# Kernel optimization log

Hardware: AMD Instinct MI355X
Metric: run time of the kernel (lower is better)

## Reference

```python
import jax, jax.numpy as jnp
import numpy as np

B, N, C, H = 8192, 36, 128, 8
HD = C // H  # 16
FOCUS = 3
EPS = 1e-4


def setup_inputs() -> dict:
    key = jax.random.key(0)
    ks = jax.random.split(key, 10)
    x = jax.random.normal(ks[0], (B, N, C), dtype=jnp.float32)
    pos = jax.random.normal(ks[1], (B, N, C), dtype=jnp.float32)
    mask = jax.random.randint(ks[2], (B, N), 0, 2).astype(jnp.float32)
    coords = jax.random.randint(ks[3], (B * N, 4), 0, 8).astype(jnp.int64)
    voxel_inds = jax.random.permutation(ks[4], B * N).reshape(B, N).astype(jnp.int64)
    s = 0.02
    qk_w = jax.random.normal(ks[5], (C, 2 * C), dtype=jnp.float32) * s
    qk_b = jnp.zeros((2 * C,), dtype=jnp.float32)
    v_w = jax.random.normal(ks[6], (C, C), dtype=jnp.float32) * s
    v_b = jnp.zeros((C,), dtype=jnp.float32)
    proj_w = jax.random.normal(ks[7], (C, C), dtype=jnp.float32) * s
    proj_b = jnp.zeros((C,), dtype=jnp.float32)
    return {"x": x, "pos": pos, "mask": mask, "qk_w": qk_w, "qk_b": qk_b,
            "v_w": v_w, "v_b": v_b, "proj_w": proj_w, "proj_b": proj_b,
            "coords": coords, "voxel_inds": voxel_inds}


def reference(x, pos, mask, qk_w, qk_b, v_w, v_b, proj_w, proj_b, coords, voxel_inds):
    b, n, c = x.shape
    qk = (x + pos) @ qk_w + qk_b                      # (B,N,2C)
    q, k = qk[..., :c], qk[..., c:]
    v = x @ v_w + v_b                                 # (B,N,C)
    k = k * mask[..., None]
    # split heads -> (B,H,N,HD)
    q = q.reshape(b, n, H, HD).transpose(0, 2, 1, 3)
    k = k.reshape(b, n, H, HD).transpose(0, 2, 1, 3)
    v = v.reshape(b, n, H, HD).transpose(0, 2, 1, 3)
    # focusing power
    q = q ** FOCUS
    k = k ** FOCUS
    # q normalized per-token over channels; k normalized per-channel over tokens
    # (original rearranges k to (bh, c, n) before norm(dim=-1))
    q = q / (EPS + jnp.linalg.norm(q, axis=-1, keepdims=True))
    k = k / (EPS + jnp.linalg.norm(k, axis=2, keepdims=True))
    # linear attention: kv = k^T v (HD x HD), then q @ kv
    kv = jnp.einsum('bhnc,bhnd->bhcd', k, v)          # (B,H,HD,HD)
    out = jnp.einsum('bhnc,bhcd->bhnd', q, kv)        # (B,H,N,HD)
    out = out.transpose(0, 2, 1, 3).reshape(b, n, c)  # (B,N,C)
    num = jnp.sum(mask, axis=-1, keepdims=True)       # (B,1)
    out = out / (num[..., None] + EPS)
    # inverse-permutation gather: perm[voxel_inds.flat] = arange
    flat = voxel_inds.reshape(-1)
    M = coords.shape[0]
    perm = jnp.zeros((M,), dtype=flat.dtype).at[flat].set(
        jnp.arange(M, dtype=flat.dtype))
    out = out.reshape(-1, c)[perm]                    # (M,C)
    out = out @ proj_w + proj_b
    return out
```

## Files before the change

kernel.cpp:

```cpp
#include <hip/hip_runtime.h>

typedef __bf16 bf16x8 __attribute__((ext_vector_type(8)));
typedef float f32x4 __attribute__((ext_vector_type(4)));

#define Bdim 8192
#define NBLK 512
#define NBATCH 16
#define Nn 36
#define Cc 128
#define EPSf 1e-4f

#define WS_QK_HI 0
#define WS_QK_LO 32768
#define WS_V_HI  65536
#define WS_P_HI  81920

#define OFF_XH   0
#define OFF_PH   12288
#define OFF_PL   24576
#define OFF_KT   36864
#define OFF_VT   50176
#define OFF_QO   63488
#define OFF_MASK 75776
#define OFF_INN  76160
#define LDS_BYTES 76288

__device__ inline uint bfh(float f) {
    __bf16 h = (__bf16)f;
    return (uint)(*(const ushort*)&h);
}
__device__ inline uint bfl(float f) {
    float hf = (float)((__bf16)f);
    __bf16 l = (__bf16)(f - hf);
    return (uint)(*(const ushort*)&l);
}
__device__ inline uint pk2h(float a, float b) { return bfh(a) | (bfh(b) << 16); }
__device__ inline uint pk2l(float a, float b) { return bfl(a) | (bfl(b) << 16); }

union U8 { bf16x8 v; uint u[4]; };

__device__ __forceinline__ void put3(char* L, int idx, float4 xv, float4 pv) {
    int n = idx >> 5, c4 = (idx & 31) << 2;
    float s0 = xv.x + pv.x, s1 = xv.y + pv.y;
    float s2 = xv.z + pv.z, s3 = xv.w + pv.w;
    uint ba = (uint)n * 256u + (((uint)(c4 * 2)) ^ (((uint)n & 15u) << 4));
    *(uint2*)(L + OFF_XH + ba) = make_uint2(pk2h(xv.x, xv.y), pk2h(xv.z, xv.w));
    *(uint2*)(L + OFF_PH + ba) = make_uint2(pk2h(s0, s1), pk2h(s2, s3));
    *(uint2*)(L + OFF_PL + ba) = make_uint2(pk2l(s0, s1), pk2l(s2, s3));
}

__device__ __forceinline__ void stage_batch(char* L, const float* __restrict__ x,
                                            const float* __restrict__ pos,
                                            const float* __restrict__ mask,
                                            int bb, int t, int wv, int lane, int pe) {
    const float* xg = x + (size_t)bb * (Nn * Cc);
    const float* pg = pos + (size_t)bb * (Nn * Cc);
    {
        int idx = t;
        int n = idx >> 5, c4 = (idx & 31) << 2;
        put3(L, idx, *(const float4*)(xg + n * Cc + c4), *(const float4*)(pg + n * Cc + c4));
    }
    {
        int idx = t + 512;
        int n = idx >> 5, c4 = (idx & 31) << 2;
        put3(L, idx, *(const float4*)(xg + n * Cc + c4), *(const float4*)(pg + n * Cc + c4));
    }
    if (t < 128) {
        int idx = t + 1024;
        int n = idx >> 5, c4 = (idx & 31) << 2;
        put3(L, idx, *(const float4*)(xg + n * Cc + c4), *(const float4*)(pg + n * Cc + c4));
    }
    float mvv = (t < Nn) ? mask[(size_t)bb * Nn + t] : 0.f;
    if (t < 48) ((float*)(L + OFF_MASK))[pe * 48 + t] = mvv;
    if (wv == 0) {
        float s = mvv;
        s += __shfl_xor(s, 1);  s += __shfl_xor(s, 2);
        s += __shfl_xor(s, 4);  s += __shfl_xor(s, 8);
        s += __shfl_xor(s, 16); s += __shfl_xor(s, 32);
        if (lane == 0) ((float*)(L + OFF_INN))[pe] = 1.f / (s + EPSf);
    }
}

__global__ __launch_bounds__(256)
void prep_frags(const float* __restrict__ qk_w, const float* __restrict__ v_w,
                const float* __restrict__ proj_w, ushort* __restrict__ ws)
{
    int e = blockIdx.x * 256 + threadIdx.x;
    const float* W; int N; int idx; int hi_off; int lo_off;
    if (e < 32768)      { W = qk_w;   N = 256; hi_off = WS_QK_HI; lo_off = WS_QK_LO; idx = e; }
    else if (e < 49152) { W = v_w;    N = 128; hi_off = WS_V_HI;  lo_off = -1;       idx = e - 32768; }
    else                { W = proj_w; N = 128; hi_off = WS_P_HI;  lo_off = -1;       idx = e - 49152; }
    int j    = idx & 7;
    int lane = (idx >> 3) & 63;
    int ks   = (idx >> 9) & 3;
    int ct   = idx >> 11;
    int col  = ct * 16 + (lane & 15);
    int k    = ks * 32 + (lane >> 4) * 8 + j;
    float v  = W[k * N + col];
    ws[hi_off + idx] = (ushort)bfh(v);
    if (lo_off >= 0) ws[lo_off + idx] = (ushort)bfl(v);
}

__global__ __launch_bounds__(512, 2)
void fla_mfma(const float* __restrict__ x, const float* __restrict__ pos,
              const float* __restrict__ mask, const float* __restrict__ qk_b,
              const float* __restrict__ v_b, const float* __restrict__ proj_b,
              const int* __restrict__ vox, const ushort* __restrict__ ws,
              float* __restrict__ out)
{
    __shared__ __align__(16) char lds[LDS_BYTES];
    const int t = threadIdx.x;
    const int lane = t & 63;
    const int wv = t >> 6;
    const int  rsel = lane & 15;
    const int  grp  = lane >> 4;
    const uint kgrp = (uint)grp * 8u;
    const uint sw   = ((uint)rsel) << 4;
    const int base = blockIdx.x * NBATCH;

    const int   c16 = wv * 16 + rsel;
    const float qb = qk_b[c16];
    const float kb = qk_b[Cc + c16];
    const float vb = v_b[c16];
    const float pb = proj_b[c16];

    stage_batch(lds, x, pos, mask, base, t, wv, lane, 0);
    __syncthreads();

    #pragma unroll 1
    for (int i = 0; i < NBATCH; ++i) {
        const int pe = i & 1;

        f32x4 accQ[3], accK[3];
        #pragma unroll
        for (int rt = 0; rt < 3; ++rt) {
            accQ[rt] = (f32x4){0.f, 0.f, 0.f, 0.f};
            accK[rt] = (f32x4){0.f, 0.f, 0.f, 0.f};
        }
        #pragma unroll
        for (int ks = 0; ks < 4; ++ks) {
            uint ka = (((uint)(ks * 32) + kgrp) * 2u) ^ sw;
            bf16x8 ph[3], pl[3];
            #pragma unroll
            for (int rt = 0; rt < 3; ++rt) {
                uint ba = (uint)(rt * 16 + rsel) * 256u + ka;
                ph[rt] = *(const bf16x8*)(lds + OFF_PH + ba);
                pl[rt] = *(const bf16x8*)(lds + OFF_PL + ba);
            }
            int fq = ((wv * 4 + ks) * 64 + lane) * 8;
            int fk = (((8 + wv) * 4 + ks) * 64 + lane) * 8;
            bf16x8 bqh = *(const bf16x8*)(ws + WS_QK_HI + fq);
            bf16x8 bql = *(const bf16x8*)(ws + WS_QK_LO + fq);
            bf16x8 bkh = *(const bf16x8*)(ws + WS_QK_HI + fk);
            bf16x8 bkl = *(const bf16x8*)(ws + WS_QK_LO + fk);
            #pragma unroll
            for (int rt = 0; rt < 3; ++rt) {
                accQ[rt] = __builtin_amdgcn_mfma_f32_16x16x32_bf16(ph[rt], bqh, accQ[rt], 0, 0, 0);
                accQ[rt] = __builtin_amdgcn_mfma_f32_16x16x32_bf16(ph[rt], bql, accQ[rt], 0, 0, 0);
                accQ[rt] = __builtin_amdgcn_mfma_f32_16x16x32_bf16(pl[rt], bqh, accQ[rt], 0, 0, 0);
                accK[rt] = __builtin_amdgcn_mfma_f32_16x16x32_bf16(ph[rt], bkh, accK[rt], 0, 0, 0);
                accK[rt] = __builtin_amdgcn_mfma_f32_16x16x32_bf16(ph[rt], bkl, accK[rt], 0, 0, 0);
                accK[rt] = __builtin_amdgcn_mfma_f32_16x16x32_bf16(pl[rt], bkh, accK[rt], 0, 0, 0);
            }
        }
        f32x4 accV[3];
        #pragma unroll
        for (int rt = 0; rt < 3; ++rt) accV[rt] = (f32x4){0.f, 0.f, 0.f, 0.f};
        #pragma unroll
        for (int ks = 0; ks < 4; ++ks) {
            uint ka = (((uint)(ks * 32) + kgrp) * 2u) ^ sw;
            bf16x8 xh[3];
            #pragma unroll
            for (int rt = 0; rt < 3; ++rt)
                xh[rt] = *(const bf16x8*)(lds + OFF_XH + (uint)(rt * 16 + rsel) * 256u + ka);
            int fv = ((wv * 4 + ks) * 64 + lane) * 8;
            bf16x8 bvh = *(const bf16x8*)(ws + WS_V_HI + fv);
            #pragma unroll
            for (int rt = 0; rt < 3; ++rt)
                accV[rt] = __builtin_amdgcn_mfma_f32_16x16x32_bf16(xh[rt], bvh, accV[rt], 0, 0, 0);
        }
        __syncthreads();

        {
            const float* sM = (const float*)(lds + OFF_MASK) + pe * 48;
            uint cb2 = (uint)(c16 * 2);
            #pragma unroll
            for (int rt = 0; rt < 3; ++rt) {
                #pragma unroll
                for (int r = 0; r < 4; ++r) {
                    int row = rt * 16 + grp * 4 + r;
                    if (row < Nn) {
                        float q1 = accQ[rt][r] + qb;
                        float q3 = q1 * q1 * q1;
                        uint ba = (uint)row * 256u + (cb2 ^ (((uint)row & 15u) << 4));
                        *(ushort*)(lds + OFF_QO + ba) = (ushort)bfh(q3);
                    }
                }
            }
            #pragma unroll
            for (int rt = 0; rt < 3; ++rt) {
                float k3v[4];
                #pragma unroll
                for (int r = 0; r < 4; ++r) {
                    int row = rt * 16 + grp * 4 + r;
                    float k1 = (accK[rt][r] + kb) * sM[row];
                    float k3 = k1 * k1 * k1;
                    k3v[r] = (rt == 2 && grp != 0) ? 0.f : k3;
                }
                uint addr = OFF_KT + (uint)(c16 * 52 + rt * 16 + grp * 4) * 2u;
                *(uint2*)(lds + addr) = make_uint2(pk2h(k3v[0], k3v[1]), pk2h(k3v[2], k3v[3]));
            }
        }
        #pragma unroll
        for (int rt = 0; rt < 3; ++rt) {
            float a0 = accV[rt][0] + vb, a1 = accV[rt][1] + vb;
            float a2 = accV[rt][2] + vb, a3 = accV[rt][3] + vb;
            if (rt == 2 && grp != 0) { a0 = 0.f; a1 = 0.f; a2 = 0.f; a3 = 0.f; }
            uint addr = OFF_VT + (uint)(c16 * 52 + rt * 16 + grp * 4) * 2u;
            *(uint2*)(lds + addr) = make_uint2(pk2h(a0, a1), pk2h(a2, a3));
        }

        if (i + 1 < NBATCH)
            stage_batch(lds, x, pos, mask, base + i + 1, t, wv, lane, pe ^ 1);

        f32x4 kvacc;
        {
            uint a0 = OFF_KT + (uint)(c16 * 52 + grp * 8) * 2u;
            uint b0 = OFF_VT + (uint)(c16 * 52 + grp * 8) * 2u;
            bf16x8 kA0 = *(const bf16x8*)(lds + a0);
            bf16x8 vB0 = *(const bf16x8*)(lds + b0);
            U8 kA1, vB1;
            kA1.u[0] = kA1.u[1] = kA1.u[2] = kA1.u[3] = 0u;
            vB1.u[0] = vB1.u[1] = vB1.u[2] = vB1.u[3] = 0u;
            if (grp < 2) {
                kA1.v = *(const bf16x8*)(lds + a0 + 64);
                vB1.v = *(const bf16x8*)(lds + b0 + 64);
            }
            float s = 0.f;
            #pragma unroll
            for (int j = 0; j < 8; ++j) { float q = (float)kA0[j]; s += q * q; }
            #pragma unroll
            for (int j = 0; j < 8; ++j) { float q = (float)kA1.v[j]; s += q * q; }
            s += __shfl_xor(s, 16);
            s += __shfl_xor(s, 32);
            float invkn = 1.f / (EPSf + sqrtf(s));

            kvacc = (f32x4){0.f, 0.f, 0.f, 0.f};
            kvacc = __builtin_amdgcn_mfma_f32_16x16x32_bf16(kA0, vB0, kvacc, 0, 0, 0);
            kvacc = __builtin_amdgcn_mfma_f32_16x16x32_bf16(kA1.v, vB1.v, kvacc, 0, 0, 0);
            #pragma unroll
            for (int r = 0; r < 4; ++r)
                kvacc[r] *= __shfl(invkn, grp * 4 + r);
        }

        {
            float bv[8];
            #pragma unroll
            for (int j = 0; j < 8; ++j)
                bv[j] = __shfl(kvacc[j & 3], rsel + 16 * (2 * grp + (j >> 2)));
            if (grp >= 2) {
                #pragma unroll
                for (int j = 0; j < 8; ++j) bv[j] = 0.f;
            }
            U8 bkv;
            bkv.u[0] = pk2h(bv[0], bv[1]); bkv.u[1] = pk2h(bv[2], bv[3]);
            bkv.u[2] = pk2h(bv[4], bv[5]); bkv.u[3] = pk2h(bv[6], bv[7]);

            float inn = ((const float*)(lds + OFF_INN))[pe];
            U8 aq[3];
            #pragma unroll
            for (int rt = 0; rt < 3; ++rt) {
                int row = rt * 16 + rsel;
                aq[rt].u[0] = aq[rt].u[1] = aq[rt].u[2] = aq[rt].u[3] = 0u;
                if (grp < 2 && row < Nn)
                    aq[rt].v = *(const bf16x8*)(lds + OFF_QO + (uint)row * 256u +
                                                (((uint)(wv * 32 + grp * 16)) ^ sw));
            }
            f32x4 oacc[3];
            float invn[3];
            #pragma unroll
            for (int rt = 0; rt < 3; ++rt) {
                float s = 0.f;
                #pragma unroll
                for (int j = 0; j < 8; ++j) { float q = (float)aq[rt].v[j]; s += q * q; }
                s += __shfl_xor(s, 16);
                invn[rt] = 1.f / (EPSf + sqrtf(s));
                f32x4 o = (f32x4){0.f, 0.f, 0.f, 0.f};
                o = __builtin_amdgcn_mfma_f32_16x16x32_bf16(aq[rt].v, bkv.v, o, 0, 0, 0);
                oacc[rt] = o;
            }
            uint cb2 = (uint)(c16 * 2);
            #pragma unroll
            for (int rt = 0; rt < 3; ++rt) {
                #pragma unroll
                for (int r = 0; r < 4; ++r) {
                    int rr = grp * 4 + r;
                    int row = rt * 16 + rr;
                    if (row < Nn) {
                        float fac = __shfl(invn[rt], rr) * inn;
                        float val = oacc[rt][r] * fac;
                        uint ba = (uint)row * 256u + (cb2 ^ (((uint)row & 15u) << 4));
                        *(ushort*)(lds + OFF_QO + ba) = (ushort)bfh(val);
                    }
                }
            }
        }
        __syncthreads();

        {
            f32x4 accP[3];
            #pragma unroll
            for (int rt = 0; rt < 3; ++rt) accP[rt] = (f32x4){0.f, 0.f, 0.f, 0.f};
            #pragma unroll
            for (int ks = 0; ks < 4; ++ks) {
                uint ka = (((uint)(ks * 32) + kgrp) * 2u) ^ sw;
                bf16x8 oa[3];
                #pragma unroll
                for (int rt = 0; rt < 3; ++rt)
                    oa[rt] = *(const bf16x8*)(lds + OFF_QO + (uint)(rt * 16 + rsel) * 256u + ka);
                int fp = ((wv * 4 + ks) * 64 + lane) * 8;
                bf16x8 bp = *(const bf16x8*)(ws + WS_P_HI + fp);
                #pragma unroll
                for (int rt = 0; rt < 3; ++rt)
                    accP[rt] = __builtin_amdgcn_mfma_f32_16x16x32_bf16(oa[rt], bp, accP[rt], 0, 0, 0);
            }
            const int* voxb = vox + (size_t)(base + i) * Nn;
            #pragma unroll
            for (int rt = 0; rt < 3; ++rt) {
                #pragma unroll
                for (int r = 0; r < 4; ++r) {
                    int row = rt * 16 + grp * 4 + r;
                    if (row < Nn)
                        out[(size_t)voxb[row] * Cc + c16] = accP[rt][r] + pb;
                }
            }
        }
    }
}

extern "C" void kernel_launch(void* const* d_in, const int* in_sizes, int n_in,
                              void* d_out, int out_size, void* d_ws, size_t ws_size,
                              hipStream_t stream) {
    (void)in_sizes; (void)n_in; (void)out_size; (void)ws_size;
    const float* x      = (const float*)d_in[0];
    const float* pos    = (const float*)d_in[1];
    const float* mask   = (const float*)d_in[2];
    const float* qk_w   = (const float*)d_in[3];
    const float* qk_b   = (const float*)d_in[4];
    const float* v_w    = (const float*)d_in[5];
    const float* v_b    = (const float*)d_in[6];
    const float* proj_w = (const float*)d_in[7];
    const float* proj_b = (const float*)d_in[8];
    const int*   vox    = (const int*)d_in[10];
    ushort* ws = (ushort*)d_ws;
    float* outp = (float*)d_out;

    hipLaunchKernelGGL(prep_frags, dim3(256), dim3(256), 0, stream, qk_w, v_w, proj_w, ws);
    hipLaunchKernelGGL(fla_mfma, dim3(NBLK), dim3(512), 0, stream,
                       x, pos, mask, qk_b, v_b, proj_b, vox, ws, outp);
}
```

Before: 251.8 us.

## Double-buffer LDS per batch, prefetch next batch into registers, hoist QK weight fragments

Splits LDS into two full per-batch buffers so the next batch's x/pos/mask global loads are issued at the top of each iteration into registers and written to the alternate buffer after the attention stage. This hides global load latency behind the QK/V MFMA work and drops one __syncthreads per iteration. QK weight fragments are loaded once into registers instead of per batch, and padding rows are zeroed once. In exchange LDS nearly doubles (about 152KB per block), which may cut occupancy below the two blocks per CU requested, and register pressure rises from the held prefetch and weight fragments.

```diff
diff --git a/kernel.cpp b/kernel.cpp
--- a/kernel.cpp
+++ b/kernel.cpp
@@ -22,8 +22,8 @@
 #define OFF_VT   50176
 #define OFF_QO   63488
 #define OFF_MASK 75776
-#define OFF_INN  76160
-#define LDS_BYTES 76288
+#define OFF_INN  75968
+#define AST      75984
 
 __device__ inline uint bfh(float f) {
     __bf16 h = (__bf16)f;
@@ -47,38 +47,6 @@
     *(uint2*)(L + OFF_XH + ba) = make_uint2(pk2h(xv.x, xv.y), pk2h(xv.z, xv.w));
     *(uint2*)(L + OFF_PH + ba) = make_uint2(pk2h(s0, s1), pk2h(s2, s3));
     *(uint2*)(L + OFF_PL + ba) = make_uint2(pk2l(s0, s1), pk2l(s2, s3));
-}
-
-__device__ __forceinline__ void stage_batch(char* L, const float* __restrict__ x,
-                                            const float* __restrict__ pos,
-                                            const float* __restrict__ mask,
-                                            int bb, int t, int wv, int lane, int pe) {
-    const float* xg = x + (size_t)bb * (Nn * Cc);
-    const float* pg = pos + (size_t)bb * (Nn * Cc);
-    {
-        int idx = t;
-        int n = idx >> 5, c4 = (idx & 31) << 2;
-        put3(L, idx, *(const float4*)(xg + n * Cc + c4), *(const float4*)(pg + n * Cc + c4));
-    }
-    {
-        int idx = t + 512;
-        int n = idx >> 5, c4 = (idx & 31) << 2;
-        put3(L, idx, *(const float4*)(xg + n * Cc + c4), *(const float4*)(pg + n * Cc + c4));
-    }
-    if (t < 128) {
-        int idx = t + 1024;
-        int n = idx >> 5, c4 = (idx & 31) << 2;
-        put3(L, idx, *(const float4*)(xg + n * Cc + c4), *(const float4*)(pg + n * Cc + c4));
-    }
-    float mvv = (t < Nn) ? mask[(size_t)bb * Nn + t] : 0.f;
-    if (t < 48) ((float*)(L + OFF_MASK))[pe * 48 + t] = mvv;
-    if (wv == 0) {
-        float s = mvv;
-        s += __shfl_xor(s, 1);  s += __shfl_xor(s, 2);
-        s += __shfl_xor(s, 4);  s += __shfl_xor(s, 8);
-        s += __shfl_xor(s, 16); s += __shfl_xor(s, 32);
-        if (lane == 0) ((float*)(L + OFF_INN))[pe] = 1.f / (s + EPSf);
-    }
 }
 
 __global__ __launch_bounds__(256)
@@ -108,7 +76,7 @@
               const int* __restrict__ vox, const ushort* __restrict__ ws,
               float* __restrict__ out)
 {
-    __shared__ __align__(16) char lds[LDS_BYTES];
+    __shared__ __align__(16) char lds[2][AST];
     const int t = threadIdx.x;
     const int lane = t & 63;
     const int wv = t >> 6;
@@ -124,12 +92,72 @@
     const float vb = v_b[c16];
     const float pb = proj_b[c16];
 
-    stage_batch(lds, x, pos, mask, base, t, wv, lane, 0);
+    bf16x8 BQH[4], BQL[4], BKH[4], BKL[4];
+    #pragma unroll
+    for (int ks = 0; ks < 4; ++ks) {
+        int fq = ((wv * 4 + ks) * 64 + lane) * 8;
+        int fk = (((8 + wv) * 4 + ks) * 64 + lane) * 8;
+        BQH[ks] = *(const bf16x8*)(ws + WS_QK_HI + fq);
+        BQL[ks] = *(const bf16x8*)(ws + WS_QK_LO + fq);
+        BKH[ks] = *(const bf16x8*)(ws + WS_QK_HI + fk);
+        BKL[ks] = *(const bf16x8*)(ws + WS_QK_LO + fk);
+    }
+
+    #pragma unroll
+    for (int z0 = 0; z0 < 3; ++z0) {
+        int z = t + z0 * 512;
+        int ar = z >= 768;
+        int zz = z & 767;
+        int reg = zz / 192;
+        int off = (zz % 192) * 16;
+        uint ro = (reg == 0) ? OFF_XH : (reg == 1) ? OFF_PH : (reg == 2) ? OFF_PL : OFF_QO;
+        *(uint4*)(lds[ar] + ro + 36 * 256 + off) = make_uint4(0u, 0u, 0u, 0u);
+    }
+
+    {
+        const float* xg = x + (size_t)base * (Nn * Cc);
+        const float* pg = pos + (size_t)base * (Nn * Cc);
+        { int n = t >> 5, c4 = (t & 31) << 2;
+          put3(lds[0], t, *(const float4*)(xg + n * Cc + c4), *(const float4*)(pg + n * Cc + c4)); }
+        { int idx = t + 512; int n = idx >> 5, c4 = (idx & 31) << 2;
+          put3(lds[0], idx, *(const float4*)(xg + n * Cc + c4), *(const float4*)(pg + n * Cc + c4)); }
+        if (t < 128) { int idx = t + 1024; int n = idx >> 5, c4 = (idx & 31) << 2;
+          put3(lds[0], idx, *(const float4*)(xg + n * Cc + c4), *(const float4*)(pg + n * Cc + c4)); }
+        float mvv = (t < Nn) ? mask[(size_t)base * Nn + t] : 0.f;
+        if (t < 48) ((float*)(lds[0] + OFF_MASK))[t] = mvv;
+        if (wv == 0) {
+            float s = mvv;
+            s += __shfl_xor(s, 1);  s += __shfl_xor(s, 2);
+            s += __shfl_xor(s, 4);  s += __shfl_xor(s, 8);
+            s += __shfl_xor(s, 16); s += __shfl_xor(s, 32);
+            if (lane == 0) *(float*)(lds[0] + OFF_INN) = 1.f / (s + EPSf);
+        }
+    }
     __syncthreads();
 
     #pragma unroll 1
     for (int i = 0; i < NBATCH; ++i) {
-        const int pe = i & 1;
+        char* L  = lds[i & 1];
+        char* Ln = lds[(i + 1) & 1];
+        const bool more = (i + 1 < NBATCH);
+
+        float4 lx0, lp0, lx1, lp1, lx2, lp2;
+        float lmv = 0.f;
+        if (more) {
+            const float* xg = x + (size_t)(base + i + 1) * (Nn * Cc);
+            const float* pg = pos + (size_t)(base + i + 1) * (Nn * Cc);
+            { int n = t >> 5, c4 = (t & 31) << 2;
+              lx0 = *(const float4*)(xg + n * Cc + c4);
+              lp0 = *(const float4*)(pg + n * Cc + c4); }
+            { int idx = t + 512; int n = idx >> 5, c4 = (idx & 31) << 2;
+              lx1 = *(const float4*)(xg + n * Cc + c4);
+              lp1 = *(const float4*)(pg + n * Cc + c4); }
+            if (t < 128) { int idx = t + 1024; int n = idx >> 5, c4 = (idx & 31) << 2;
+              lx2 = *(const float4*)(xg + n * Cc + c4);
+              lp2 = *(const float4*)(pg + n * Cc + c4); }
+            lmv = (t < Nn) ? mask[(size_t)(base + i + 1) * Nn + t] : 0.f;
+        }
+        __builtin_amdgcn_sched_barrier(0);
 
         f32x4 accQ[3], accK[3];
         #pragma unroll
@@ -144,23 +172,17 @@
             #pragma unroll
             for (int rt = 0; rt < 3; ++rt) {
                 uint ba = (uint)(rt * 16 + rsel) * 256u + ka;
-                ph[rt] = *(const bf16x8*)(lds + OFF_PH + ba);
-                pl[rt] = *(const bf16x8*)(lds + OFF_PL + ba);
-            }
-            int fq = ((wv * 4 + ks) * 64 + lane) * 8;
-            int fk = (((8 + wv) * 4 + ks) * 64 + lane) * 8;
-            bf16x8 bqh = *(const bf16x8*)(ws + WS_QK_HI + fq);
-            bf16x8 bql = *(const bf16x8*)(ws + WS_QK_LO + fq);
-            bf16x8 bkh = *(const bf16x8*)(ws + WS_QK_HI + fk);
-            bf16x8 bkl = *(const bf16x8*)(ws + WS_QK_LO + fk);
-            #pragma unroll
-            for (int rt = 0; rt < 3; ++rt) {
-                accQ[rt] = __builtin_amdgcn_mfma_f32_16x16x32_bf16(ph[rt], bqh, accQ[rt], 0, 0, 0);
-                accQ[rt] = __builtin_amdgcn_mfma_f32_16x16x32_bf16(ph[rt], bql, accQ[rt], 0, 0, 0);
-                accQ[rt] = __builtin_amdgcn_mfma_f32_16x16x32_bf16(pl[rt], bqh, accQ[rt], 0, 0, 0);
-                accK[rt] = __builtin_amdgcn_mfma_f32_16x16x32_bf16(ph[rt], bkh, accK[rt], 0, 0, 0);
-                accK[rt] = __builtin_amdgcn_mfma_f32_16x16x32_bf16(ph[rt], bkl, accK[rt], 0, 0, 0);
-                accK[rt] = __builtin_amdgcn_mfma_f32_16x16x32_bf16(pl[rt], bkh, accK[rt], 0, 0, 0);
+                ph[rt] = *(const bf16x8*)(L + OFF_PH + ba);
+                pl[rt] = *(const bf16x8*)(L + OFF_PL + ba);
+            }
+            #pragma unroll
+            for (int rt = 0; rt < 3; ++rt) {
+                accQ[rt] = __builtin_amdgcn_mfma_f32_16x16x32_bf16(ph[rt], BQH[ks], accQ[rt], 0, 0, 0);
+                accQ[rt] = __builtin_amdgcn_mfma_f32_16x16x32_bf16(ph[rt], BQL[ks], accQ[rt], 0, 0, 0);
+                accQ[rt] = __builtin_amdgcn_mfma_f32_16x16x32_bf16(pl[rt], BQH[ks], accQ[rt], 0, 0, 0);
+                accK[rt] = __builtin_amdgcn_mfma_f32_16x16x32_bf16(ph[rt], BKH[ks], accK[rt], 0, 0, 0);
+                accK[rt] = __builtin_amdgcn_mfma_f32_16x16x32_bf16(ph[rt], BKL[ks], accK[rt], 0, 0, 0);
+                accK[rt] = __builtin_amdgcn_mfma_f32_16x16x32_bf16(pl[rt], BKH[ks], accK[rt], 0, 0, 0);
             }
         }
         f32x4 accV[3];
@@ -172,17 +194,16 @@
             bf16x8 xh[3];
             #pragma unroll
             for (int rt = 0; rt < 3; ++rt)
-                xh[rt] = *(const bf16x8*)(lds + OFF_XH + (uint)(rt * 16 + rsel) * 256u + ka);
+                xh[rt] = *(const bf16x8*)(L + OFF_XH + (uint)(rt * 16 + rsel) * 256u + ka);
             int fv = ((wv * 4 + ks) * 64 + lane) * 8;
             bf16x8 bvh = *(const bf16x8*)(ws + WS_V_HI + fv);
             #pragma unroll
             for (int rt = 0; rt < 3; ++rt)
                 accV[rt] = __builtin_amdgcn_mfma_f32_16x16x32_bf16(xh[rt], bvh, accV[rt], 0, 0, 0);
         }
-        __syncthreads();
 
         {
-            const float* sM = (const float*)(lds + OFF_MASK) + pe * 48;
+            const float* sM = (const float*)(L + OFF_MASK);
             uint cb2 = (uint)(c16 * 2);
             #pragma unroll
             for (int rt = 0; rt < 3; ++rt) {
@@ -193,7 +214,7 @@
                         float q1 = accQ[rt][r] + qb;
                         float q3 = q1 * q1 * q1;
                         uint ba = (uint)row * 256u + (cb2 ^ (((uint)row & 15u) << 4));
-                        *(ushort*)(lds + OFF_QO + ba) = (ushort)bfh(q3);
+                        *(ushort*)(L + OFF_QO + ba) = (ushort)bfh(q3);
                     }
                 }
             }
@@ -208,7 +229,7 @@
                     k3v[r] = (rt == 2 && grp != 0) ? 0.f : k3;
                 }
                 uint addr = OFF_KT + (uint)(c16 * 52 + rt * 16 + grp * 4) * 2u;
-                *(uint2*)(lds + addr) = make_uint2(pk2h(k3v[0], k3v[1]), pk2h(k3v[2], k3v[3]));
+                *(uint2*)(L + addr) = make_uint2(pk2h(k3v[0], k3v[1]), pk2h(k3v[2], k3v[3]));
             }
         }
         #pragma unroll
@@ -217,24 +238,21 @@
             float a2 = accV[rt][2] + vb, a3 = accV[rt][3] + vb;
             if (rt == 2 && grp != 0) { a0 = 0.f; a1 = 0.f; a2 = 0.f; a3 = 0.f; }
             uint addr = OFF_VT + (uint)(c16 * 52 + rt * 16 + grp * 4) * 2u;
-            *(uint2*)(lds + addr) = make_uint2(pk2h(a0, a1), pk2h(a2, a3));
-        }
-
-        if (i + 1 < NBATCH)
-            stage_batch(lds, x, pos, mask, base + i + 1, t, wv, lane, pe ^ 1);
+            *(uint2*)(L + addr) = make_uint2(pk2h(a0, a1), pk2h(a2, a3));
+        }
 
         f32x4 kvacc;
         {
             uint a0 = OFF_KT + (uint)(c16 * 52 + grp * 8) * 2u;
             uint b0 = OFF_VT + (uint)(c16 * 52 + grp * 8) * 2u;
-            bf16x8 kA0 = *(const bf16x8*)(lds + a0);
-            bf16x8 vB0 = *(const bf16x8*)(lds + b0);
+            bf16x8 kA0 = *(const bf16x8*)(L + a0);
+            bf16x8 vB0 = *(const bf16x8*)(L + b0);
             U8 kA1, vB1;
             kA1.u[0] = kA1.u[1] = kA1.u[2] = kA1.u[3] = 0u;
             vB1.u[0] = vB1.u[1] = vB1.u[2] = vB1.u[3] = 0u;
             if (grp < 2) {
-                kA1.v = *(const bf16x8*)(lds + a0 + 64);
-                vB1.v = *(const bf16x8*)(lds + b0 + 64);
+                kA1.v = *(const bf16x8*)(L + a0 + 64);
+                vB1.v = *(const bf16x8*)(L + b0 + 64);
             }
             float s = 0.f;
             #pragma unroll
@@ -266,14 +284,14 @@
             bkv.u[0] = pk2h(bv[0], bv[1]); bkv.u[1] = pk2h(bv[2], bv[3]);
             bkv.u[2] = pk2h(bv[4], bv[5]); bkv.u[3] = pk2h(bv[6], bv[7]);
 
-            float inn = ((const float*)(lds + OFF_INN))[pe];
+            float inn = *(const float*)(L + OFF_INN);
             U8 aq[3];
             #pragma unroll
             for (int rt = 0; rt < 3; ++rt) {
                 int row = rt * 16 + rsel;
                 aq[rt].u[0] = aq[rt].u[1] = aq[rt].u[2] = aq[rt].u[3] = 0u;
                 if (grp < 2 && row < Nn)
-                    aq[rt].v = *(const bf16x8*)(lds + OFF_QO + (uint)row * 256u +
+                    aq[rt].v = *(const bf16x8*)(L + OFF_QO + (uint)row * 256u +
                                                 (((uint)(wv * 32 + grp * 16)) ^ sw));
             }
             f32x4 oacc[3];
@@ -300,9 +318,23 @@
                         float fac = __shfl(invn[rt], rr) * inn;
                         float val = oacc[rt][r] * fac;
                         uint ba = (uint)row * 256u + (cb2 ^ (((uint)row & 15u) << 4));
-                        *(ushort*)(lds + OFF_QO + ba) = (ushort)bfh(val);
+                        *(ushort*)(L + OFF_QO + ba) = (ushort)bfh(val);
                     }
                 }
+            }
+        }
+
+        if (more) {
+            put3(Ln, t, lx0, lp0);
+            put3(Ln, t + 512, lx1, lp1);
+            if (t < 128) put3(Ln, t + 1024, lx2, lp2);
+            if (t < 48) ((float*)(Ln + OFF_MASK))[t] = lmv;
+            if (wv == 0) {
+                float s = lmv;
+                s += __shfl_xor(s, 1);  s += __shfl_xor(s, 2);
+                s += __shfl_xor(s, 4);  s += __shfl_xor(s, 8);
+                s += __shfl_xor(s, 16); s += __shfl_xor(s, 32);
+                if (lane == 0) *(float*)(Ln + OFF_INN) = 1.f / (s + EPSf);
             }
         }
         __syncthreads();
@@ -317,7 +349,7 @@
                 bf16x8 oa[3];
                 #pragma unroll
                 for (int rt = 0; rt < 3; ++rt)
-                    oa[rt] = *(const bf16x8*)(lds + OFF_QO + (uint)(rt * 16 + rsel) * 256u + ka);
+                    oa[rt] = *(const bf16x8*)(L + OFF_QO + (uint)(rt * 16 + rsel) * 256u + ka);
                 int fp = ((wv * 4 + ks) * 64 + lane) * 8;
                 bf16x8 bp = *(const bf16x8*)(ws + WS_P_HI + fp);
                 #pragma unroll
```

Measured after the change: 228.6 us. -9.2%, faster.

## Process two batches per block with interleaved stages and smaller aliased LDS

Applied to the files above, without the earlier changes.

Replaces the 512-block persistent loop over 16 batches with 4096 blocks that each handle two batches. Work is split into stage lambdas that are interleaved across the two batches, so one batch's MFMA work overlaps the other's staging and epilogue. The LDS regions for the staged inputs and the K/V/Q buffers now alias, which roughly halves shared memory per batch and lets launch bounds request 4 blocks per CU. The cost is more blocks, each reloading weight fragments, and register pressure from holding two sets of accumulators.

```diff
diff --git a/kernel.cpp b/kernel.cpp
--- a/kernel.cpp
+++ b/kernel.cpp
@@ -4,8 +4,6 @@
 typedef float f32x4 __attribute__((ext_vector_type(4)));
 
 #define Bdim 8192
-#define NBLK 512
-#define NBATCH 16
 #define Nn 36
 #define Cc 128
 #define EPSf 1e-4f
@@ -18,12 +16,12 @@
 #define OFF_XH   0
 #define OFF_PH   12288
 #define OFF_PL   24576
-#define OFF_KT   36864
-#define OFF_VT   50176
-#define OFF_QO   63488
-#define OFF_MASK 75776
-#define OFF_INN  76160
-#define LDS_BYTES 76288
+#define OFF_KT   0
+#define OFF_VT   13312
+#define OFF_QO   26624
+#define OFF_MASK 38912
+#define OFF_INN  39104
+#define AST      39168
 
 __device__ inline uint bfh(float f) {
     __bf16 h = (__bf16)f;
@@ -38,48 +36,6 @@
 __device__ inline uint pk2l(float a, float b) { return bfl(a) | (bfl(b) << 16); }
 
 union U8 { bf16x8 v; uint u[4]; };
-
-__device__ __forceinline__ void put3(char* L, int idx, float4 xv, float4 pv) {
-    int n = idx >> 5, c4 = (idx & 31) << 2;
-    float s0 = xv.x + pv.x, s1 = xv.y + pv.y;
-    float s2 = xv.z + pv.z, s3 = xv.w + pv.w;
-    uint ba = (uint)n * 256u + (((uint)(c4 * 2)) ^ (((uint)n & 15u) << 4));
-    *(uint2*)(L + OFF_XH + ba) = make_uint2(pk2h(xv.x, xv.y), pk2h(xv.z, xv.w));
-    *(uint2*)(L + OFF_PH + ba) = make_uint2(pk2h(s0, s1), pk2h(s2, s3));
-    *(uint2*)(L + OFF_PL + ba) = make_uint2(pk2l(s0, s1), pk2l(s2, s3));
-}
-
-__device__ __forceinline__ void stage_batch(char* L, const float* __restrict__ x,
-                                            const float* __restrict__ pos,
-                                            const float* __restrict__ mask,
-                                            int bb, int t, int wv, int lane, int pe) {
-    const float* xg = x + (size_t)bb * (Nn * Cc);
-    const float* pg = pos + (size_t)bb * (Nn * Cc);
-    {
-        int idx = t;
-        int n = idx >> 5, c4 = (idx & 31) << 2;
-        put3(L, idx, *(const float4*)(xg + n * Cc + c4), *(const float4*)(pg + n * Cc + c4));
-    }
-    {
-        int idx = t + 512;
-        int n = idx >> 5, c4 = (idx & 31) << 2;
-        put3(L, idx, *(const float4*)(xg + n * Cc + c4), *(const float4*)(pg + n * Cc + c4));
-    }
-    if (t < 128) {
-        int idx = t + 1024;
-        int n = idx >> 5, c4 = (idx & 31) << 2;
-        put3(L, idx, *(const float4*)(xg + n * Cc + c4), *(const float4*)(pg + n * Cc + c4));
-    }
-    float mvv = (t < Nn) ? mask[(size_t)bb * Nn + t] : 0.f;
-    if (t < 48) ((float*)(L + OFF_MASK))[pe * 48 + t] = mvv;
-    if (wv == 0) {
-        float s = mvv;
-        s += __shfl_xor(s, 1);  s += __shfl_xor(s, 2);
-        s += __shfl_xor(s, 4);  s += __shfl_xor(s, 8);
-        s += __shfl_xor(s, 16); s += __shfl_xor(s, 32);
-        if (lane == 0) ((float*)(L + OFF_INN))[pe] = 1.f / (s + EPSf);
-    }
-}
 
 __global__ __launch_bounds__(256)
 void prep_frags(const float* __restrict__ qk_w, const float* __restrict__ v_w,
@@ -101,14 +57,14 @@
     if (lo_off >= 0) ws[lo_off + idx] = (ushort)bfl(v);
 }
 
-__global__ __launch_bounds__(512, 2)
+__global__ __launch_bounds__(512, 4)
 void fla_mfma(const float* __restrict__ x, const float* __restrict__ pos,
               const float* __restrict__ mask, const float* __restrict__ qk_b,
               const float* __restrict__ v_b, const float* __restrict__ proj_b,
               const int* __restrict__ vox, const ushort* __restrict__ ws,
               float* __restrict__ out)
 {
-    __shared__ __align__(16) char lds[LDS_BYTES];
+    __shared__ __align__(16) char lds[2][AST];
     const int t = threadIdx.x;
     const int lane = t & 63;
     const int wv = t >> 6;
@@ -116,7 +72,9 @@
     const int  grp  = lane >> 4;
     const uint kgrp = (uint)grp * 8u;
     const uint sw   = ((uint)rsel) << 4;
-    const int base = blockIdx.x * NBATCH;
+
+    const int b0 = blockIdx.x * 2;
+    const int b1 = b0 + 1;
 
     const int   c16 = wv * 16 + rsel;
     const float qb = qk_b[c16];
@@ -124,18 +82,42 @@
     const float vb = v_b[c16];
     const float pb = proj_b[c16];
 
-    stage_batch(lds, x, pos, mask, base, t, wv, lane, 0);
-    __syncthreads();
-
-    #pragma unroll 1
-    for (int i = 0; i < NBATCH; ++i) {
-        const int pe = i & 1;
-
-        f32x4 accQ[3], accK[3];
+    auto PA = [&](int ar, int bb) {
+        char* L = lds[ar];
+        const float* xg = x + (size_t)bb * (Nn * Cc);
+        const float* pg = pos + (size_t)bb * (Nn * Cc);
+        auto put = [&](int idx) {
+            int n = idx >> 5, c4 = (idx & 31) << 2;
+            float4 xv = *(const float4*)(xg + n * Cc + c4);
+            float4 pv = *(const float4*)(pg + n * Cc + c4);
+            float s0 = xv.x + pv.x, s1 = xv.y + pv.y;
+            float s2 = xv.z + pv.z, s3 = xv.w + pv.w;
+            uint ba = (uint)n * 256u + (((uint)(c4 * 2)) ^ (((uint)n & 15u) << 4));
+            *(uint2*)(L + OFF_XH + ba) = make_uint2(pk2h(xv.x, xv.y), pk2h(xv.z, xv.w));
+            *(uint2*)(L + OFF_PH + ba) = make_uint2(pk2h(s0, s1), pk2h(s2, s3));
+            *(uint2*)(L + OFF_PL + ba) = make_uint2(pk2l(s0, s1), pk2l(s2, s3));
+        };
+        put(t);
+        put(t + 512);
+        if (t < 128) put(t + 1024);
+        float mvv = (t < Nn) ? mask[(size_t)bb * Nn + t] : 0.f;
+        if (t < 48) ((float*)(L + OFF_MASK))[t] = mvv;
+        if (wv == 0) {
+            float s = mvv;
+            s += __shfl_xor(s, 1);  s += __shfl_xor(s, 2);
+            s += __shfl_xor(s, 4);  s += __shfl_xor(s, 8);
+            s += __shfl_xor(s, 16); s += __shfl_xor(s, 32);
+            if (lane == 0) *(float*)(L + OFF_INN) = 1.f / (s + EPSf);
+        }
+    };
+
+    auto PB = [&](int ar, f32x4 (&accQ)[3], f32x4 (&accK)[3], f32x4 (&accV)[3]) {
+        char* L = lds[ar];
         #pragma unroll
         for (int rt = 0; rt < 3; ++rt) {
             accQ[rt] = (f32x4){0.f, 0.f, 0.f, 0.f};
             accK[rt] = (f32x4){0.f, 0.f, 0.f, 0.f};
+            accV[rt] = (f32x4){0.f, 0.f, 0.f, 0.f};
         }
         #pragma unroll
         for (int ks = 0; ks < 4; ++ks) {
@@ -144,8 +126,8 @@
             #pragma unroll
             for (int rt = 0; rt < 3; ++rt) {
                 uint ba = (uint)(rt * 16 + rsel) * 256u + ka;
-                ph[rt] = *(const bf16x8*)(lds + OFF_PH + ba);
-                pl[rt] = *(const bf16x8*)(lds + OFF_PL + ba);
+                ph[rt] = *(const bf16x8*)(L + OFF_PH + ba);
+                pl[rt] = *(const bf16x8*)(L + OFF_PL + ba);
             }
             int fq = ((wv * 4 + ks) * 64 + lane) * 8;
             int fk = (((8 + wv) * 4 + ks) * 64 + lane) * 8;
@@ -163,53 +145,50 @@
                 accK[rt] = __builtin_amdgcn_mfma_f32_16x16x32_bf16(pl[rt], bkh, accK[rt], 0, 0, 0);
             }
         }
-        f32x4 accV[3];
-        #pragma unroll
-        for (int rt = 0; rt < 3; ++rt) accV[rt] = (f32x4){0.f, 0.f, 0.f, 0.f};
         #pragma unroll
         for (int ks = 0; ks < 4; ++ks) {
             uint ka = (((uint)(ks * 32) + kgrp) * 2u) ^ sw;
             bf16x8 xh[3];
             #pragma unroll
             for (int rt = 0; rt < 3; ++rt)
-                xh[rt] = *(const bf16x8*)(lds + OFF_XH + (uint)(rt * 16 + rsel) * 256u + ka);
+                xh[rt] = *(const bf16x8*)(L + OFF_XH + (uint)(rt * 16 + rsel) * 256u + ka);
             int fv = ((wv * 4 + ks) * 64 + lane) * 8;
             bf16x8 bvh = *(const bf16x8*)(ws + WS_V_HI + fv);
             #pragma unroll
             for (int rt = 0; rt < 3; ++rt)
                 accV[rt] = __builtin_amdgcn_mfma_f32_16x16x32_bf16(xh[rt], bvh, accV[rt], 0, 0, 0);
         }
-        __syncthreads();
-
-        {
-            const float* sM = (const float*)(lds + OFF_MASK) + pe * 48;
-            uint cb2 = (uint)(c16 * 2);
-            #pragma unroll
-            for (int rt = 0; rt < 3; ++rt) {
-                #pragma unroll
-                for (int r = 0; r < 4; ++r) {
-                    int row = rt * 16 + grp * 4 + r;
-                    if (row < Nn) {
-                        float q1 = accQ[rt][r] + qb;
-                        float q3 = q1 * q1 * q1;
-                        uint ba = (uint)row * 256u + (cb2 ^ (((uint)row & 15u) << 4));
-                        *(ushort*)(lds + OFF_QO + ba) = (ushort)bfh(q3);
-                    }
+    };
+
+    auto PC = [&](int ar, f32x4 (&accQ)[3], f32x4 (&accK)[3], f32x4 (&accV)[3]) {
+        char* L = lds[ar];
+        const float* sM = (const float*)(L + OFF_MASK);
+        uint cb2 = (uint)(c16 * 2);
+        #pragma unroll
+        for (int rt = 0; rt < 3; ++rt) {
+            #pragma unroll
+            for (int r = 0; r < 4; ++r) {
+                int row = rt * 16 + grp * 4 + r;
+                if (row < Nn) {
+                    float q1 = accQ[rt][r] + qb;
+                    float q3 = q1 * q1 * q1;
+                    uint ba = (uint)row * 256u + (cb2 ^ (((uint)row & 15u) << 4));
+                    *(ushort*)(L + OFF_QO + ba) = (ushort)bfh(q3);
                 }
             }
-            #pragma unroll
-            for (int rt = 0; rt < 3; ++rt) {
-                float k3v[4];
-                #pragma unroll
-                for (int r = 0; r < 4; ++r) {
-                    int row = rt * 16 + grp * 4 + r;
-                    float k1 = (accK[rt][r] + kb) * sM[row];
-                    float k3 = k1 * k1 * k1;
-                    k3v[r] = (rt == 2 && grp != 0) ? 0.f : k3;
-                }
-                uint addr = OFF_KT + (uint)(c16 * 52 + rt * 16 + grp * 4) * 2u;
-                *(uint2*)(lds + addr) = make_uint2(pk2h(k3v[0], k3v[1]), pk2h(k3v[2], k3v[3]));
-            }
+        }
+        #pragma unroll
+        for (int rt = 0; rt < 3; ++rt) {
+            float k3v[4];
+            #pragma unroll
+            for (int r = 0; r < 4; ++r) {
+                int row = rt * 16 + grp * 4 + r;
+                float k1 = (accK[rt][r] + kb) * sM[row];
+                float k3 = k1 * k1 * k1;
+                k3v[r] = (rt == 2 && grp != 0) ? 0.f : k3;
+            }
+            uint addr = OFF_KT + (uint)(c16 * 52 + rt * 16 + grp * 4) * 2u;
+            *(uint2*)(L + addr) = make_uint2(pk2h(k3v[0], k3v[1]), pk2h(k3v[2], k3v[3]));
         }
         #pragma unroll
         for (int rt = 0; rt < 3; ++rt) {
@@ -217,24 +196,24 @@
             float a2 = accV[rt][2] + vb, a3 = accV[rt][3] + vb;
             if (rt == 2 && grp != 0) { a0 = 0.f; a1 = 0.f; a2 = 0.f; a3 = 0.f; }
             uint addr = OFF_VT + (uint)(c16 * 52 + rt * 16 + grp * 4) * 2u;
-            *(uint2*)(lds + addr) = make_uint2(pk2h(a0, a1), pk2h(a2, a3));
-        }
-
-        if (i + 1 < NBATCH)
-            stage_batch(lds, x, pos, mask, base + i + 1, t, wv, lane, pe ^ 1);
-
+            *(uint2*)(L + addr) = make_uint2(pk2h(a0, a1), pk2h(a2, a3));
+        }
+    };
+
+    auto PDE = [&](int ar) {
+        char* L = lds[ar];
         f32x4 kvacc;
         {
             uint a0 = OFF_KT + (uint)(c16 * 52 + grp * 8) * 2u;
-            uint b0 = OFF_VT + (uint)(c16 * 52 + grp * 8) * 2u;
-            bf16x8 kA0 = *(const bf16x8*)(lds + a0);
-            bf16x8 vB0 = *(const bf16x8*)(lds + b0);
+            uint b0_ = OFF_VT + (uint)(c16 * 52 + grp * 8) * 2u;
+            bf16x8 kA0 = *(const bf16x8*)(L + a0);
+            bf16x8 vB0 = *(const bf16x8*)(L + b0_);
             U8 kA1, vB1;
             kA1.u[0] = kA1.u[1] = kA1.u[2] = kA1.u[3] = 0u;
             vB1.u[0] = vB1.u[1] = vB1.u[2] = vB1.u[3] = 0u;
             if (grp < 2) {
-                kA1.v = *(const bf16x8*)(lds + a0 + 64);
-                vB1.v = *(const bf16x8*)(lds + b0 + 64);
+                kA1.v = *(const bf16x8*)(L + a0 + 64);
+                vB1.v = *(const bf16x8*)(L + b0_ + 64);
             }
             float s = 0.f;
             #pragma unroll
@@ -252,7 +231,6 @@
             for (int r = 0; r < 4; ++r)
                 kvacc[r] *= __shfl(invkn, grp * 4 + r);
         }
-
         {
             float bv[8];
             #pragma unroll
@@ -266,14 +244,14 @@
             bkv.u[0] = pk2h(bv[0], bv[1]); bkv.u[1] = pk2h(bv[2], bv[3]);
             bkv.u[2] = pk2h(bv[4], bv[5]); bkv.u[3] = pk2h(bv[6], bv[7]);
 
-            float inn = ((const float*)(lds + OFF_INN))[pe];
+            float inn = *(const float*)(L + OFF_INN);
             U8 aq[3];
             #pragma unroll
             for (int rt = 0; rt < 3; ++rt) {
                 int row = rt * 16 + rsel;
                 aq[rt].u[0] = aq[rt].u[1] = aq[rt].u[2] = aq[rt].u[3] = 0u;
                 if (grp < 2 && row < Nn)
-                    aq[rt].v = *(const bf16x8*)(lds + OFF_QO + (uint)row * 256u +
+                    aq[rt].v = *(const bf16x8*)(L + OFF_QO + (uint)row * 256u +
                                                 (((uint)(wv * 32 + grp * 16)) ^ sw));
             }
             f32x4 oacc[3];
@@ -300,42 +278,61 @@
                         float fac = __shfl(invn[rt], rr) * inn;
                         float val = oacc[rt][r] * fac;
                         uint ba = (uint)row * 256u + (cb2 ^ (((uint)row & 15u) << 4));
-                        *(ushort*)(lds + OFF_QO + ba) = (ushort)bfh(val);
+                        *(ushort*)(L + OFF_QO + ba) = (ushort)bfh(val);
                     }
                 }
             }
         }
-        __syncthreads();
-
-        {
-            f32x4 accP[3];
-            #pragma unroll
-            for (int rt = 0; rt < 3; ++rt) accP[rt] = (f32x4){0.f, 0.f, 0.f, 0.f};
-            #pragma unroll
-            for (int ks = 0; ks < 4; ++ks) {
-                uint ka = (((uint)(ks * 32) + kgrp) * 2u) ^ sw;
-                bf16x8 oa[3];
-                #pragma unroll
-                for (int rt = 0; rt < 3; ++rt)
-                    oa[rt] = *(const bf16x8*)(lds + OFF_QO + (uint)(rt * 16 + rsel) * 256u + ka);
-                int fp = ((wv * 4 + ks) * 64 + lane) * 8;
-                bf16x8 bp = *(const bf16x8*)(ws + WS_P_HI + fp);
-                #pragma unroll
-                for (int rt = 0; rt < 3; ++rt)
-                    accP[rt] = __builtin_amdgcn_mfma_f32_16x16x32_bf16(oa[rt], bp, accP[rt], 0, 0, 0);
-            }
-            const int* voxb = vox + (size_t)(base + i) * Nn;
-            #pragma unroll
-            for (int rt = 0; rt < 3; ++rt) {
-                #pragma unroll
-                for (int r = 0; r < 4; ++r) {
-                    int row = rt * 16 + grp * 4 + r;
-                    if (row < Nn)
-                        out[(size_t)voxb[row] * Cc + c16] = accP[rt][r] + pb;
-                }
-            }
-        }
-    }
+    };
+
+    auto PG = [&](int ar, int bb) {
+        char* L = lds[ar];
+        f32x4 accP[3];
+        #pragma unroll
+        for (int rt = 0; rt < 3; ++rt) accP[rt] = (f32x4){0.f, 0.f, 0.f, 0.f};
+        #pragma unroll
+        for (int ks = 0; ks < 4; ++ks) {
+            uint ka = (((uint)(ks * 32) + kgrp) * 2u) ^ sw;
+            bf16x8 oa[3];
+            #pragma unroll
+            for (int rt = 0; rt < 3; ++rt)
+                oa[rt] = *(const bf16x8*)(L + OFF_QO + (uint)(rt * 16 + rsel) * 256u + ka);
+            int fp = ((wv * 4 + ks) * 64 + lane) * 8;
+            bf16x8 bp = *(const bf16x8*)(ws + WS_P_HI + fp);
+            #pragma unroll
+            for (int rt = 0; rt < 3; ++rt)
+                accP[rt] = __builtin_amdgcn_mfma_f32_16x16x32_bf16(oa[rt], bp, accP[rt], 0, 0, 0);
+        }
+        const int* voxb = vox + (size_t)bb * Nn;
+        #pragma unroll
+        for (int rt = 0; rt < 3; ++rt) {
+            #pragma unroll
+            for (int r = 0; r < 4; ++r) {
+                int row = rt * 16 + grp * 4 + r;
+                if (row < Nn)
+                    out[(size_t)voxb[row] * Cc + c16] = accP[rt][r] + pb;
+            }
+        }
+    };
+
+    f32x4 aQ0[3], aK0[3], aV0[3];
+    f32x4 aQ1[3], aK1[3], aV1[3];
+
+    PA(0, b0);
+    __syncthreads();
+    PB(0, aQ0, aK0, aV0);
+    PA(1, b1);
+    __syncthreads();
+    PC(0, aQ0, aK0, aV0);
+    PB(1, aQ1, aK1, aV1);
+    __syncthreads();
+    PDE(0);
+    PC(1, aQ1, aK1, aV1);
+    __syncthreads();
+    PG(0, b0);
+    PDE(1);
+    __syncthreads();
+    PG(1, b1);
 }
 
 extern "C" void kernel_launch(void* const* d_in, const int* in_sizes, int n_in,
@@ -356,6 +353,6 @@
     float* outp = (float*)d_out;
 
     hipLaunchKernelGGL(prep_frags, dim3(256), dim3(256), 0, stream, qk_w, v_w, proj_w, ws);
-    hipLaunchKernelGGL(fla_mfma, dim3(NBLK), dim3(512), 0, stream,
+    hipLaunchKernelGGL(fla_mfma, dim3(Bdim / 2), dim3(512), 0, stream,
                        x, pos, mask, qk_b, v_b, proj_b, vox, ws, outp);
 }
```

Result: faster. 224.5 us (-10.8%).
